# Performance work log

Measured on AMD Instinct MI355X. Metric: run time of the kernel, lower is better.

The kernel has to match this reference:

```python
import jax, jax.numpy as jnp
import numpy as np

N_NODES = 50000
N_EDGES = 800000
IN_C, HID_C, OUT_C = 128, 256, 128


def _gcn_conv(x, src, dst, W, b, num_nodes):
    # PyG GCNConv: self-loops + symmetric normalization + linear + scatter-add
    deg = jax.ops.segment_sum(jnp.ones_like(src, x.dtype), dst, num_segments=num_nodes)
    dinv = jnp.where(deg > 0, jax.lax.rsqrt(deg), 0.0)
    norm = dinv[src] * dinv[dst]                      # [E']
    h = x @ W.T                                       # [N, C_out] transform first (C_out usually < C_in path cost)
    msg = h[src] * norm[:, None]                      # [E', C_out] gather + scale
    out = jax.ops.segment_sum(msg, dst, num_segments=num_nodes)  # scatter-add
    return out + b


def setup_inputs() -> dict:
    key = jax.random.key(0)
    k1, k2, k3, k4 = jax.random.split(key, 4)
    x = jax.random.normal(k1, (N_NODES, IN_C), dtype=jnp.float32)
    edge_index = jax.random.randint(k2, (2, N_EDGES), 0, N_NODES, dtype=jnp.int64)
    W1 = jax.random.normal(k3, (HID_C, IN_C), dtype=jnp.float32) * (1.0 / np.sqrt(IN_C))
    b1 = jnp.zeros((HID_C,), dtype=jnp.float32)
    W2 = jax.random.normal(k4, (OUT_C, HID_C), dtype=jnp.float32) * (1.0 / np.sqrt(HID_C))
    b2 = jnp.zeros((OUT_C,), dtype=jnp.float32)
    return {"x": x, "edge_index": edge_index, "W1": W1, "b1": b1,
            "W2": W2, "b2": b2, "num_nodes": N_NODES}


def reference(x, edge_index, W1, b1, W2, b2, num_nodes):
    # add self-loops once (shared by both layers)
    loop = jnp.arange(num_nodes, dtype=edge_index.dtype)
    src = jnp.concatenate([edge_index[0], loop])
    dst = jnp.concatenate([edge_index[1], loop])
    h = _gcn_conv(x, src, dst, W1, b1, num_nodes)
    h = jax.nn.relu(h)
    out = _gcn_conv(h, src, dst, W2, b2, num_nodes)
    return out
```

## Files before the change

### kernel.cpp

```cpp
#include <hip/hip_runtime.h>

#define N_NODES 50000
#define N_EDGES 800000
#define IN_C 128
#define HID_C 256
#define OUT_C 128
#define NBLK 196
#define NPART 8
#define PART_W 6250
#define KB2 32
#define CHUNK (N_EDGES / KB2)
#define EB 3125
#define XCONV_BLKS 6250
#define WCONV_BLKS 64

typedef __attribute__((ext_vector_type(8))) short short8v;
typedef __attribute__((ext_vector_type(4))) float f32x4;

static __device__ __forceinline__ unsigned short f2bf(float f) {
  unsigned int u = __float_as_uint(f);
  unsigned int r = (u + 0x7fffu + ((u >> 16) & 1u)) >> 16;
  return (unsigned short)r;
}
static __device__ __forceinline__ float bf2f(unsigned short h) {
  return __uint_as_float(((unsigned int)h) << 16);
}
static __device__ __forceinline__ unsigned int packBF2(float a, float b) {
  return (unsigned int)f2bf(a) | ((unsigned int)f2bf(b) << 16);
}

__global__ __launch_bounds__(256) void convert_conv_k(
    const int* __restrict__ ei, unsigned int* __restrict__ edata,
    const float* __restrict__ x, unsigned int* __restrict__ xbf,
    const float* __restrict__ W1, unsigned int* __restrict__ w1bf,
    const float* __restrict__ W2, unsigned int* __restrict__ w2bf) {
  const int b = blockIdx.x;
  if (b < EB) {
    __shared__ int s_is64;
    if (threadIdx.x == 0) {
      int nz = 0;
#pragma unroll
      for (int k = 0; k < 64; ++k) nz |= ei[2 * k + 1];
      s_is64 = (nz == 0) ? 1 : 0;
    }
    __syncthreads();
    const int is64 = s_is64;
    const int e = b * 256 + threadIdx.x;
    if (e < N_EDGES) {
      int s, d;
      if (is64) {
        const uint2 sv = ((const uint2*)ei)[e];
        const uint2 dv = ((const uint2*)ei)[N_EDGES + e];
        s = (int)sv.x;
        d = (int)dv.x;
      } else {
        s = ei[e];
        d = ei[N_EDGES + e];
      }
      edata[e] = (unsigned int)d | ((unsigned int)s << 16);
    }
  } else if (b < EB + XCONV_BLKS) {
    const int i = (b - EB) * 256 + threadIdx.x;
    const float4 f = *(const float4*)(x + (long)i * 4);
    uint2 u = {packBF2(f.x, f.y), packBF2(f.z, f.w)};
    *(uint2*)(xbf + (long)i * 2) = u;
  } else if (b < EB + XCONV_BLKS + WCONV_BLKS) {
    const int i = (b - EB - XCONV_BLKS) * 256 + threadIdx.x;
    const float2 f = *(const float2*)(W1 + (long)i * 2);
    w1bf[i] = packBF2(f.x, f.y);
  } else {
    const int i = (b - EB - XCONV_BLKS - WCONV_BLKS) * 256 + threadIdx.x;
    const float2 f = *(const float2*)(W2 + (long)i * 2);
    w2bf[i] = packBF2(f.x, f.y);
  }
}

__global__ __launch_bounds__(1024) void hist_k(const unsigned int* __restrict__ edata,
                                               int* __restrict__ H) {
  const int p = blockIdx.x & 7;
  const int c = blockIdx.x >> 3;
  __shared__ unsigned int hist[PART_W];
  for (int i = threadIdx.x; i < PART_W; i += 1024) hist[i] = 0;
  __syncthreads();
  const int s0 = c * CHUNK;
  for (int i = s0 + threadIdx.x; i < s0 + CHUNK; i += 1024) {
    const unsigned int u = edata[i];
    const int d = (int)(u & 0xffffu);
    if (d / PART_W == p) atomicAdd(&hist[d - p * PART_W], 1u);
  }
  __syncthreads();
  int* Hrow = H + (p * KB2 + c) * PART_W;
  for (int i = threadIdx.x; i < PART_W; i += 1024) Hrow[i] = (int)hist[i];
}

__global__ __launch_bounds__(256) void bsum_k(const int* __restrict__ H,
                                              int* __restrict__ bsum) {
  const int i = blockIdx.x * 256 + threadIdx.x;
  int v = 0;
  if (i < N_NODES) {
    const int p = i / PART_W, bin = i % PART_W;
    const int* Hp = H + p * KB2 * PART_W + bin;
#pragma unroll
    for (int c = 0; c < KB2; ++c) v += Hp[c * PART_W];
  }
#pragma unroll
  for (int off = 32; off > 0; off >>= 1) v += __shfl_down(v, off, 64);
  __shared__ int ws[4];
  if ((threadIdx.x & 63) == 0) ws[threadIdx.x >> 6] = v;
  __syncthreads();
  if (threadIdx.x == 0) bsum[blockIdx.x] = ws[0] + ws[1] + ws[2] + ws[3];
}

__global__ __launch_bounds__(256) void bscan_k(const int* __restrict__ bsum,
                                               int* __restrict__ boff) {
  __shared__ int s[256];
  const int t = threadIdx.x;
  const int v = (t < NBLK) ? bsum[t] : 0;
  s[t] = v;
  __syncthreads();
  for (int off = 1; off < 256; off <<= 1) {
    const int tmp = (t >= off) ? s[t - off] : 0;
    __syncthreads();
    s[t] += tmp;
    __syncthreads();
  }
  if (t < NBLK) boff[t] = s[t] - v;
}

__global__ __launch_bounds__(256) void bfinal_k(int* __restrict__ H,
                                                const int* __restrict__ boff,
                                                int* __restrict__ rowstart,
                                                float* __restrict__ dinv) {
  __shared__ int s[256];
  const int t = threadIdx.x;
  const int i = blockIdx.x * 256 + t;
  int dtot = 0;
  int p = 0, bin = 0;
  if (i < N_NODES) {
    p = i / PART_W;
    bin = i % PART_W;
    int* Hp = H + p * KB2 * PART_W + bin;
#pragma unroll
    for (int c = 0; c < KB2; ++c) dtot += Hp[c * PART_W];
  }
  s[t] = dtot;
  __syncthreads();
  for (int off = 1; off < 256; off <<= 1) {
    const int tmp = (t >= off) ? s[t - off] : 0;
    __syncthreads();
    s[t] += tmp;
    __syncthreads();
  }
  const int run = boff[blockIdx.x] + s[t] - dtot;
  if (i < N_NODES) {
    rowstart[i] = run;
    dinv[i] = rsqrtf((float)dtot + 1.0f);
    int acc = run;
    int* Hp = H + p * KB2 * PART_W + bin;
#pragma unroll
    for (int c = 0; c < KB2; ++c) {
      const int cnt = Hp[c * PART_W];
      Hp[c * PART_W] = acc;
      acc += cnt;
    }
    if (i == N_NODES - 1) rowstart[N_NODES] = run + dtot;
  }
}

__global__ __launch_bounds__(1024) void scatter_k(const unsigned int* __restrict__ edata,
                                                  const int* __restrict__ H,
                                                  int* __restrict__ csr_src) {
  const int p = blockIdx.x & 7;
  const int c = blockIdx.x >> 3;
  __shared__ unsigned int hist[PART_W];
  for (int i = threadIdx.x; i < PART_W; i += 1024) hist[i] = 0;
  __syncthreads();
  const int s0 = c * CHUNK;
  const int* Hrow = H + (p * KB2 + c) * PART_W;
  for (int i = s0 + threadIdx.x; i < s0 + CHUNK; i += 1024) {
    const unsigned int u = edata[i];
    const int d = (int)(u & 0xffffu);
    if (d / PART_W == p) {
      const int ld = d - p * PART_W;
      const int lr = (int)atomicAdd(&hist[ld], 1u);
      csr_src[Hrow[ld] + lr] = (int)(u >> 16);
    }
  }
}

__global__ __launch_bounds__(256) void gemm_fused_k(
    const unsigned int* __restrict__ X,
    const unsigned int* __restrict__ W1BF,
    const float* __restrict__ b1,
    const unsigned int* __restrict__ W2BF,
    unsigned int* __restrict__ outBF) {
  constexpr int KP1 = 68;
  constexpr int HP = 132;
  __shared__ unsigned int xs[64 * KP1];
  __shared__ unsigned int h1s[64 * HP];

  const int tid = threadIdx.x;
  const int w = tid >> 6;
  const int l = tid & 63;
  const long nbase = (long)blockIdx.x * 64;
  const int kg = (l >> 4) * 8;
  const int lr = l & 15;
  const int mq0 = (l >> 4) * 4;

#pragma unroll
  for (int i = 0; i < 4; ++i) {
    const int idx = (tid + i * 256) * 4;
    const int row = idx >> 6, col = idx & 63;
    long gr = nbase + row;
    if (gr > N_NODES - 1) gr = N_NODES - 1;
    const uint4 v = *(const uint4*)(X + gr * 64 + col);
    *(uint4*)(xs + row * KP1 + col) = v;
  }
  __syncthreads();

  {
    const int m0w = w * 64;
    f32x4 acc[4][4];
#pragma unroll
    for (int nt = 0; nt < 4; ++nt)
#pragma unroll
      for (int mt = 0; mt < 4; ++mt) acc[nt][mt] = {0.0f, 0.0f, 0.0f, 0.0f};

#pragma unroll
    for (int ks = 0; ks < 4; ++ks) {
      const int ko = ks * 32 + kg;
      short8v wb[4];
#pragma unroll
      for (int mt = 0; mt < 4; ++mt)
        wb[mt] = *(const short8v*)(W1BF + (long)(m0w + mt * 16 + lr) * (IN_C / 2) +
                                   ko / 2);
#pragma unroll
      for (int nt = 0; nt < 4; ++nt) {
        const short8v xb = *(const short8v*)(xs + (nt * 16 + lr) * KP1 + ko / 2);
#pragma unroll
        for (int mt = 0; mt < 4; ++mt)
          acc[nt][mt] = __builtin_amdgcn_mfma_f32_16x16x32_bf16(wb[mt], xb,
                                                               acc[nt][mt], 0, 0, 0);
      }
    }

#pragma unroll
    for (int nt = 0; nt < 4; ++nt) {
      const int nl = nt * 16 + lr;
#pragma unroll
      for (int mt = 0; mt < 4; ++mt) {
        const int mq = m0w + mt * 16 + mq0;
        const float4 bv = *(const float4*)(b1 + mq);
        const float v0 = fmaxf(acc[nt][mt][0] + bv.x, 0.0f);
        const float v1 = fmaxf(acc[nt][mt][1] + bv.y, 0.0f);
        const float v2 = fmaxf(acc[nt][mt][2] + bv.z, 0.0f);
        const float v3 = fmaxf(acc[nt][mt][3] + bv.w, 0.0f);
        uint2 o = {packBF2(v0, v1), packBF2(v2, v3)};
        *(uint2*)(h1s + nl * HP + mq / 2) = o;
      }
    }
  }
  __syncthreads();

  {
    const int m0w = w * 32;
    f32x4 acc[4][2];
#pragma unroll
    for (int nt = 0; nt < 4; ++nt)
#pragma unroll
      for (int mt = 0; mt < 2; ++mt) acc[nt][mt] = {0.0f, 0.0f, 0.0f, 0.0f};

#pragma unroll
    for (int ks = 0; ks < 8; ++ks) {
      const int ko = ks * 32 + kg;
      short8v wb[2];
#pragma unroll
      for (int mt = 0; mt < 2; ++mt)
        wb[mt] = *(const short8v*)(W2BF + (long)(m0w + mt * 16 + lr) * (HID_C / 2) +
                                   ko / 2);
#pragma unroll
      for (int nt = 0; nt < 4; ++nt) {
        const short8v xb = *(const short8v*)(h1s + (nt * 16 + lr) * HP + ko / 2);
#pragma unroll
        for (int mt = 0; mt < 2; ++mt)
          acc[nt][mt] = __builtin_amdgcn_mfma_f32_16x16x32_bf16(wb[mt], xb,
                                                               acc[nt][mt], 0, 0, 0);
      }
    }

#pragma unroll
    for (int nt = 0; nt < 4; ++nt) {
      const long n = nbase + nt * 16 + lr;
      if (n < N_NODES) {
#pragma unroll
        for (int mt = 0; mt < 2; ++mt) {
          const int mq = m0w + mt * 16 + mq0;
          uint2 o = {packBF2(acc[nt][mt][0], acc[nt][mt][1]),
                     packBF2(acc[nt][mt][2], acc[nt][mt][3])};
          *(uint2*)(outBF + n * (OUT_C / 2) + mq / 2) = o;
        }
      }
    }
  }
}

template <int C, bool HAS_BIAS, bool OUT_BF>
__global__ __launch_bounds__(256) void gather_k(const int* __restrict__ rowstart,
                                                const int* __restrict__ csr_src,
                                                const float* __restrict__ dinv,
                                                const unsigned int* __restrict__ hbf,
                                                const float* __restrict__ bias,
                                                float* __restrict__ out,
                                                unsigned int* __restrict__ outBF) {
  const int v = (blockIdx.x * 256 + threadIdx.x) >> 6;
  if (v >= N_NODES) return;
  const int lane = threadIdx.x & 63;
  constexpr int CW = C / 2;
  const int rs = rowstart[v];
  const int re = rowstart[v + 1];
  const float dv = dinv[v];

  float a0 = 0.0f, a1 = 0.0f;

  int e = rs;
  for (; e + 7 < re; e += 8) {
    int s[8];
    float nn[8];
    unsigned int r[8];
#pragma unroll
    for (int j = 0; j < 8; ++j) s[j] = csr_src[e + j];
#pragma unroll
    for (int j = 0; j < 8; ++j) nn[j] = dv * dinv[s[j]];
#pragma unroll
    for (int j = 0; j < 8; ++j) r[j] = hbf[(long)s[j] * CW + lane];
#pragma unroll
    for (int j = 0; j < 8; ++j) {
      a0 += nn[j] * bf2f((unsigned short)r[j]);
      a1 += nn[j] * bf2f((unsigned short)(r[j] >> 16));
    }
  }
  for (; e + 3 < re; e += 4) {
    int s[4];
    float nn[4];
    unsigned int r[4];
#pragma unroll
    for (int j = 0; j < 4; ++j) s[j] = csr_src[e + j];
#pragma unroll
    for (int j = 0; j < 4; ++j) nn[j] = dv * dinv[s[j]];
#pragma unroll
    for (int j = 0; j < 4; ++j) r[j] = hbf[(long)s[j] * CW + lane];
#pragma unroll
    for (int j = 0; j < 4; ++j) {
      a0 += nn[j] * bf2f((unsigned short)r[j]);
      a1 += nn[j] * bf2f((unsigned short)(r[j] >> 16));
    }
  }
  for (; e < re; ++e) {
    const int s0 = csr_src[e];
    const float n0 = dv * dinv[s0];
    const unsigned int r0 = hbf[(long)s0 * CW + lane];
    a0 += n0 * bf2f((unsigned short)r0);
    a1 += n0 * bf2f((unsigned short)(r0 >> 16));
  }

  const float s2 = dv * dv;
  const unsigned int hv = hbf[(long)v * CW + lane];
  float o0 = s2 * bf2f((unsigned short)hv) + a0;
  float o1 = s2 * bf2f((unsigned short)(hv >> 16)) + a1;
  if (HAS_BIAS) {
    const float2 bv = *(const float2*)(bias + lane * 2);
    o0 += bv.x;
    o1 += bv.y;
  }
  if (OUT_BF) {
    outBF[(long)v * CW + lane] = packBF2(o0, o1);
  } else {
    const float2 o = {o0, o1};
    *(float2*)(out + (long)v * CW * 2 + lane * 2) = o;
  }
}

extern "C" void kernel_launch(void* const* d_in, const int* in_sizes, int n_in,
                              void* d_out, int out_size, void* d_ws, size_t ws_size,
                              hipStream_t stream) {
  (void)in_sizes; (void)n_in; (void)out_size; (void)ws_size;

  const float* x  = (const float*)d_in[0];
  const int*   ei = (const int*)d_in[1];
  const float* W1 = (const float*)d_in[2];
  const float* b1 = (const float*)d_in[3];
  const float* W2 = (const float*)d_in[4];
  const float* b2 = (const float*)d_in[5];
  float* out = (float*)d_out;

  char* ws = (char*)d_ws;
  unsigned int* edata = (unsigned int*)(ws + 0);
  int*   csr_src  = (int*)(ws + 3200000);
  int*   H        = (int*)(ws + 6400000);
  int*   rowstart = (int*)(ws + 12800000);
  float* dinv     = (float*)(ws + 13000512);
  int*   bsum     = (int*)(ws + 13200512);
  int*   boff     = (int*)(ws + 13201536);
  unsigned int* w1bf   = (unsigned int*)(ws + 13300000);
  unsigned int* w2bf   = (unsigned int*)(ws + 13400000);
  unsigned int* aggxbf = (unsigned int*)(ws + 14000000);
  unsigned int* h2bf   = (unsigned int*)(ws + 27000000);
  unsigned int* xbf    = (unsigned int*)(ws + 91200000);

  const int GB = (N_NODES + 3) / 4;

  convert_conv_k<<<EB + XCONV_BLKS + 2 * WCONV_BLKS, 256, 0, stream>>>(
      ei, edata, x, xbf, W1, w1bf, W2, w2bf);
  hist_k<<<NPART * KB2, 1024, 0, stream>>>(edata, H);
  bsum_k<<<NBLK, 256, 0, stream>>>(H, bsum);
  bscan_k<<<1, 256, 0, stream>>>(bsum, boff);
  bfinal_k<<<NBLK, 256, 0, stream>>>(H, boff, rowstart, dinv);
  scatter_k<<<NPART * KB2, 1024, 0, stream>>>(edata, H, csr_src);

  gather_k<IN_C, false, true><<<GB, 256, 0, stream>>>(
      rowstart, csr_src, dinv, xbf, nullptr, nullptr, aggxbf);

  gemm_fused_k<<<(N_NODES + 63) / 64, 256, 0, stream>>>(aggxbf, w1bf, b1, w2bf,
                                                        h2bf);

  gather_k<OUT_C, true, false><<<GB, 256, 0, stream>>>(
      rowstart, csr_src, dinv, h2bf, b2, out, nullptr);
}
```

Before: 153.1 us.

## Prescale features by source dinv to drop per-edge norm gathers

Factors the symmetric normalization so rows are pre-multiplied by dinv[src]. The x conversion moves into the scatter kernel, after dinv exists, and the first GEMM epilogue scales its output by dinv. The gather kernels then sum raw rows and apply dinv[dst] once per node, which removes the dependent per-edge dinv[s] load and multiply, and the inner loop is unrolled to 16 edges for more memory-level parallelism. The trade-off is that the x conversion now waits behind the CSR build instead of overlapping the edge conversion, and the register count in the gather goes up.

```diff
diff --git a/kernel.cpp b/kernel.cpp
--- a/kernel.cpp
+++ b/kernel.cpp
@@ -11,8 +11,8 @@
 #define KB2 32
 #define CHUNK (N_EDGES / KB2)
 #define EB 3125
-#define XCONV_BLKS 6250
-#define WCONV_BLKS 64
+#define SC_SCAT 256
+#define SC_XC 1563
 
 typedef __attribute__((ext_vector_type(8))) short short8v;
 typedef __attribute__((ext_vector_type(4))) float f32x4;
@@ -29,11 +29,12 @@
   return (unsigned int)f2bf(a) | ((unsigned int)f2bf(b) << 16);
 }
 
-__global__ __launch_bounds__(256) void convert_conv_k(
-    const int* __restrict__ ei, unsigned int* __restrict__ edata,
-    const float* __restrict__ x, unsigned int* __restrict__ xbf,
-    const float* __restrict__ W1, unsigned int* __restrict__ w1bf,
-    const float* __restrict__ W2, unsigned int* __restrict__ w2bf) {
+__global__ __launch_bounds__(256) void convert_k(const int* __restrict__ ei,
+                                                 unsigned int* __restrict__ edata,
+                                                 const float* __restrict__ W1,
+                                                 unsigned int* __restrict__ w1bf,
+                                                 const float* __restrict__ W2,
+                                                 unsigned int* __restrict__ w2bf) {
   const int b = blockIdx.x;
   if (b < EB) {
     __shared__ int s_is64;
@@ -59,17 +60,12 @@
       }
       edata[e] = (unsigned int)d | ((unsigned int)s << 16);
     }
-  } else if (b < EB + XCONV_BLKS) {
+  } else if (b < EB + 64) {
     const int i = (b - EB) * 256 + threadIdx.x;
-    const float4 f = *(const float4*)(x + (long)i * 4);
-    uint2 u = {packBF2(f.x, f.y), packBF2(f.z, f.w)};
-    *(uint2*)(xbf + (long)i * 2) = u;
-  } else if (b < EB + XCONV_BLKS + WCONV_BLKS) {
-    const int i = (b - EB - XCONV_BLKS) * 256 + threadIdx.x;
     const float2 f = *(const float2*)(W1 + (long)i * 2);
     w1bf[i] = packBF2(f.x, f.y);
   } else {
-    const int i = (b - EB - XCONV_BLKS - WCONV_BLKS) * 256 + threadIdx.x;
+    const int i = (b - EB - 64) * 256 + threadIdx.x;
     const float2 f = *(const float2*)(W2 + (long)i * 2);
     w2bf[i] = packBF2(f.x, f.y);
   }
@@ -167,23 +163,36 @@
   }
 }
 
-__global__ __launch_bounds__(1024) void scatter_k(const unsigned int* __restrict__ edata,
-                                                  const int* __restrict__ H,
-                                                  int* __restrict__ csr_src) {
-  const int p = blockIdx.x & 7;
-  const int c = blockIdx.x >> 3;
-  __shared__ unsigned int hist[PART_W];
-  for (int i = threadIdx.x; i < PART_W; i += 1024) hist[i] = 0;
-  __syncthreads();
-  const int s0 = c * CHUNK;
-  const int* Hrow = H + (p * KB2 + c) * PART_W;
-  for (int i = s0 + threadIdx.x; i < s0 + CHUNK; i += 1024) {
-    const unsigned int u = edata[i];
-    const int d = (int)(u & 0xffffu);
-    if (d / PART_W == p) {
-      const int ld = d - p * PART_W;
-      const int lr = (int)atomicAdd(&hist[ld], 1u);
-      csr_src[Hrow[ld] + lr] = (int)(u >> 16);
+__global__ __launch_bounds__(1024) void scatter_xconv_k(
+    const unsigned int* __restrict__ edata, const int* __restrict__ H,
+    int* __restrict__ csr_src, const float* __restrict__ x,
+    const float* __restrict__ dinv, unsigned int* __restrict__ xbf) {
+  const int b = blockIdx.x;
+  if (b < SC_SCAT) {
+    const int p = b & 7;
+    const int c = b >> 3;
+    __shared__ unsigned int hist[PART_W];
+    for (int i = threadIdx.x; i < PART_W; i += 1024) hist[i] = 0;
+    __syncthreads();
+    const int s0 = c * CHUNK;
+    const int* Hrow = H + (p * KB2 + c) * PART_W;
+    for (int i = s0 + threadIdx.x; i < s0 + CHUNK; i += 1024) {
+      const unsigned int u = edata[i];
+      const int d = (int)(u & 0xffffu);
+      if (d / PART_W == p) {
+        const int ld = d - p * PART_W;
+        const int lr = (int)atomicAdd(&hist[ld], 1u);
+        csr_src[Hrow[ld] + lr] = (int)(u >> 16);
+      }
+    }
+  } else {
+    const int i = (b - SC_SCAT) * 1024 + threadIdx.x;
+    if (i < N_NODES * IN_C / 4) {
+      const int v = i >> 5;
+      const float dv = dinv[v];
+      const float4 f = *(const float4*)(x + (long)i * 4);
+      uint2 u = {packBF2(dv * f.x, dv * f.y), packBF2(dv * f.z, dv * f.w)};
+      *(uint2*)(xbf + (long)i * 2) = u;
     }
   }
 }
@@ -193,6 +202,7 @@
     const unsigned int* __restrict__ W1BF,
     const float* __restrict__ b1,
     const unsigned int* __restrict__ W2BF,
+    const float* __restrict__ dinv,
     unsigned int* __restrict__ outBF) {
   constexpr int KP1 = 68;
   constexpr int HP = 132;
@@ -292,11 +302,12 @@
     for (int nt = 0; nt < 4; ++nt) {
       const long n = nbase + nt * 16 + lr;
       if (n < N_NODES) {
+        const float dvn = dinv[n];
 #pragma unroll
         for (int mt = 0; mt < 2; ++mt) {
           const int mq = m0w + mt * 16 + mq0;
-          uint2 o = {packBF2(acc[nt][mt][0], acc[nt][mt][1]),
-                     packBF2(acc[nt][mt][2], acc[nt][mt][3])};
+          uint2 o = {packBF2(dvn * acc[nt][mt][0], dvn * acc[nt][mt][1]),
+                     packBF2(dvn * acc[nt][mt][2], dvn * acc[nt][mt][3])};
           *(uint2*)(outBF + n * (OUT_C / 2) + mq / 2) = o;
         }
       }
@@ -323,50 +334,54 @@
   float a0 = 0.0f, a1 = 0.0f;
 
   int e = rs;
+  for (; e + 15 < re; e += 16) {
+    int s[16];
+    unsigned int r[16];
+#pragma unroll
+    for (int j = 0; j < 16; ++j) s[j] = csr_src[e + j];
+#pragma unroll
+    for (int j = 0; j < 16; ++j) r[j] = hbf[(long)s[j] * CW + lane];
+#pragma unroll
+    for (int j = 0; j < 16; ++j) {
+      a0 += bf2f((unsigned short)r[j]);
+      a1 += bf2f((unsigned short)(r[j] >> 16));
+    }
+  }
   for (; e + 7 < re; e += 8) {
     int s[8];
-    float nn[8];
     unsigned int r[8];
 #pragma unroll
     for (int j = 0; j < 8; ++j) s[j] = csr_src[e + j];
 #pragma unroll
-    for (int j = 0; j < 8; ++j) nn[j] = dv * dinv[s[j]];
-#pragma unroll
     for (int j = 0; j < 8; ++j) r[j] = hbf[(long)s[j] * CW + lane];
 #pragma unroll
     for (int j = 0; j < 8; ++j) {
-      a0 += nn[j] * bf2f((unsigned short)r[j]);
-      a1 += nn[j] * bf2f((unsigned short)(r[j] >> 16));
+      a0 += bf2f((unsigned short)r[j]);
+      a1 += bf2f((unsigned short)(r[j] >> 16));
     }
   }
   for (; e + 3 < re; e += 4) {
     int s[4];
-    float nn[4];
     unsigned int r[4];
 #pragma unroll
     for (int j = 0; j < 4; ++j) s[j] = csr_src[e + j];
 #pragma unroll
-    for (int j = 0; j < 4; ++j) nn[j] = dv * dinv[s[j]];
-#pragma unroll
     for (int j = 0; j < 4; ++j) r[j] = hbf[(long)s[j] * CW + lane];
 #pragma unroll
     for (int j = 0; j < 4; ++j) {
-      a0 += nn[j] * bf2f((unsigned short)r[j]);
-      a1 += nn[j] * bf2f((unsigned short)(r[j] >> 16));
+      a0 += bf2f((unsigned short)r[j]);
+      a1 += bf2f((unsigned short)(r[j] >> 16));
     }
   }
   for (; e < re; ++e) {
-    const int s0 = csr_src[e];
-    const float n0 = dv * dinv[s0];
-    const unsigned int r0 = hbf[(long)s0 * CW + lane];
-    a0 += n0 * bf2f((unsigned short)r0);
-    a1 += n0 * bf2f((unsigned short)(r0 >> 16));
-  }
-
-  const float s2 = dv * dv;
+    const unsigned int r0 = hbf[(long)csr_src[e] * CW + lane];
+    a0 += bf2f((unsigned short)r0);
+    a1 += bf2f((unsigned short)(r0 >> 16));
+  }
+
   const unsigned int hv = hbf[(long)v * CW + lane];
-  float o0 = s2 * bf2f((unsigned short)hv) + a0;
-  float o1 = s2 * bf2f((unsigned short)(hv >> 16)) + a1;
+  float o0 = dv * (a0 + bf2f((unsigned short)hv));
+  float o1 = dv * (a1 + bf2f((unsigned short)(hv >> 16)));
   if (HAS_BIAS) {
     const float2 bv = *(const float2*)(bias + lane * 2);
     o0 += bv.x;
@@ -409,19 +424,19 @@
 
   const int GB = (N_NODES + 3) / 4;
 
-  convert_conv_k<<<EB + XCONV_BLKS + 2 * WCONV_BLKS, 256, 0, stream>>>(
-      ei, edata, x, xbf, W1, w1bf, W2, w2bf);
+  convert_k<<<EB + 128, 256, 0, stream>>>(ei, edata, W1, w1bf, W2, w2bf);
   hist_k<<<NPART * KB2, 1024, 0, stream>>>(edata, H);
   bsum_k<<<NBLK, 256, 0, stream>>>(H, bsum);
   bscan_k<<<1, 256, 0, stream>>>(bsum, boff);
   bfinal_k<<<NBLK, 256, 0, stream>>>(H, boff, rowstart, dinv);
-  scatter_k<<<NPART * KB2, 1024, 0, stream>>>(edata, H, csr_src);
+  scatter_xconv_k<<<SC_SCAT + SC_XC, 1024, 0, stream>>>(edata, H, csr_src, x,
+                                                        dinv, xbf);
 
   gather_k<IN_C, false, true><<<GB, 256, 0, stream>>>(
       rowstart, csr_src, dinv, xbf, nullptr, nullptr, aggxbf);
 
   gemm_fused_k<<<(N_NODES + 63) / 64, 256, 0, stream>>>(aggxbf, w1bf, b1, w2bf,
-                                                        h2bf);
+                                                        dinv, h2bf);
 
   gather_k<OUT_C, true, false><<<GB, 256, 0, stream>>>(
       rowstart, csr_src, dinv, h2bf, b2, out, nullptr);
```

New measurement: 148.5 us, median of 2. 1.03x faster.
